# Kernel tuning notes

Hardware: AMD Instinct MI355X
Metric: run time of the kernel (lower is better)

The kernel has to match this reference:

```python
import jax, jax.numpy as jnp
import numpy as np

T, N, E = 336, 3233, 20000
FEAT, D, H = 14, 64, 128


def setup_inputs() -> dict:
    key = jax.random.key(0)
    ks = jax.random.split(key, 12)
    s = lambda k, shape, fan: jax.random.normal(k, shape, jnp.float32) / np.sqrt(fan)
    return {
        "x": jax.random.normal(ks[0], (T, N, FEAT), jnp.float32),
        "edge_index": jax.random.randint(ks[1], (2, E), 0, N, jnp.int64 if jax.config.jax_enable_x64 else jnp.int32),
        "edge_weight": jax.random.uniform(ks[2], (E,), jnp.float32),
        "W1": s(ks[3], (FEAT, D), FEAT), "b1": jnp.zeros((D,), jnp.float32),
        "W2": s(ks[4], (D, D), D), "b2": jnp.zeros((D,), jnp.float32),
        "county_bias": s(ks[5], (N, D), D),
        "W_ih": s(ks[6], (4 * H, D), D), "W_hh": s(ks[7], (4 * H, H), H),
        "b_ih": jnp.zeros((4 * H,), jnp.float32), "b_hh": jnp.zeros((4 * H,), jnp.float32),
        "Wm1": s(ks[8], (H, H // 2), H), "bm1": jnp.zeros((H // 2,), jnp.float32),
        "Wm2": s(ks[9], (H // 2, 1), H // 2), "bm2": jnp.zeros((1,), jnp.float32),
    }


def _gcn_norm(edge_index, edge_weight, n):
    # PyG GCNConv: add self-loops (weight 1) + symmetric normalization
    loop = jnp.arange(n, dtype=edge_index.dtype)
    src = jnp.concatenate([edge_index[0], loop])
    dst = jnp.concatenate([edge_index[1], loop])
    w = jnp.concatenate([edge_weight, jnp.ones((n,), edge_weight.dtype)])
    deg = jax.ops.segment_sum(w, dst, num_segments=n)
    dis = jnp.where(deg > 0, jax.lax.rsqrt(jnp.where(deg > 0, deg, 1.0)), 0.0)
    return src, dst, dis[src] * w * dis[dst]


def _gcn(h, src, dst, norm, W, b):
    # h: [T,N,Fin] -> [T,N,Fout]; transform then gather-scale-scatter over edges
    hw = jnp.einsum("tnf,fd->tnd", h, W)
    msg = hw[:, src, :] * norm[None, :, None]          # [T,E',Fout]
    out = jnp.zeros_like(hw).at[:, dst, :].add(msg)
    return out + b


def reference(x, edge_index, edge_weight, W1, b1, W2, b2, county_bias,
              W_ih, W_hh, b_ih, b_hh, Wm1, bm1, Wm2, bm2):
    n = x.shape[1]
    src, dst, norm = _gcn_norm(edge_index, edge_weight, n)
    h = jax.nn.relu(_gcn(x, src, dst, norm, W1, b1))
    embeds = _gcn(h, src, dst, norm, W2, b2) + county_bias[None]  # [T,N,D]

    hid = W_hh.shape[1]
    def step(carry, x_t):  # x_t: [N,D]
        hprev, cprev = carry
        g = x_t @ W_ih.T + hprev @ W_hh.T + (b_ih + b_hh)
        i, f, gg, o = jnp.split(g, 4, axis=-1)
        c = jax.nn.sigmoid(f) * cprev + jax.nn.sigmoid(i) * jnp.tanh(gg)
        hh = jax.nn.sigmoid(o) * jnp.tanh(c)
        return (hh, c), None

    init = (jnp.zeros((n, hid), x.dtype), jnp.zeros((n, hid), x.dtype))
    (h_final, _), _ = jax.lax.scan(step, init, embeds)
    z = jax.nn.relu(h_final @ Wm1 + bm1)
    return (z @ Wm2 + bm2)[:, 0]
```

## Files before the change

kernel.cpp:

```cpp
#include <hip/hip_runtime.h>
#include <math.h>


#define T_DIM 336
#define N_DIM 3233
#define E_DIM 20000
#define FEAT  14
#define D_DIM 64
#define H_DIM 128
#define ET    (E_DIM + N_DIM)

typedef _Float16 f16;
typedef _Float16 half8_t __attribute__((ext_vector_type(8)));
typedef _Float16 half2_t __attribute__((ext_vector_type(2)));
typedef float float4_t __attribute__((ext_vector_type(4)));

__device__ __forceinline__ float sigf(float x) {
    return __builtin_amdgcn_rcpf(1.f + exp2f(-1.4426950408889634f * x));
}
__device__ __forceinline__ float tanhfast(float x) {
    return 1.f - 2.f * __builtin_amdgcn_rcpf(1.f + exp2f(2.8853900817779268f * x));
}


__global__ void k_init(int* cnt, int* fill) {
    int i = blockIdx.x * 256 + threadIdx.x;
    if (i < N_DIM) { cnt[i] = 0; fill[i] = 0; }
}

__global__ void k_cnt(const int* __restrict__ ei, int* cnt) {
    int e = blockIdx.x * 256 + threadIdx.x;
    if (e < E_DIM) atomicAdd(&cnt[ei[E_DIM + e]], 1);
}

__global__ void k_scan(const int* __restrict__ cnt, int* __restrict__ rowp) {
    __shared__ int csum[1024];
    int tid = threadIdx.x;
    int base = tid * 4;
    int v[4];
    int s = 0;
    #pragma unroll
    for (int m = 0; m < 4; m++) {
        int idx = base + m;
        int len = (idx < N_DIM) ? (cnt[idx] + 1) : 0;
        v[m] = s; s += len;
    }
    csum[tid] = s;
    __syncthreads();
    for (int off = 1; off < 1024; off <<= 1) {
        int t2 = (tid >= off) ? csum[tid - off] : 0;
        __syncthreads();
        csum[tid] += t2;
        __syncthreads();
    }
    int pre = (tid > 0) ? csum[tid - 1] : 0;
    #pragma unroll
    for (int m = 0; m < 4; m++) {
        int idx = base + m;
        if (idx <= N_DIM) rowp[idx] = pre + v[m];
    }
}

__global__ void k_fill(const int* __restrict__ ei, const int* __restrict__ rowp,
                       int* fill, int* __restrict__ eid) {
    int e = blockIdx.x * 256 + threadIdx.x;
    if (e < ET) {
        int d = (e < E_DIM) ? ei[E_DIM + e] : (e - E_DIM);
        int p = rowp[d] + atomicAdd(&fill[d], 1);
        eid[p] = e;
    }
}

__global__ void k_sortdeg(const float* __restrict__ ew, const int* __restrict__ rowp,
                          int* __restrict__ eid, float* __restrict__ dis) {
    int n = blockIdx.x * 256 + threadIdx.x;
    if (n >= N_DIM) return;
    int p0 = rowp[n], p1 = rowp[n + 1];
    for (int i = p0 + 1; i < p1; i++) {
        int key = eid[i];
        int j = i - 1;
        while (j >= p0 && eid[j] > key) { eid[j + 1] = eid[j]; j--; }
        eid[j + 1] = key;
    }
    float deg = 0.f;
    for (int p = p0; p < p1; p++) {
        int e = eid[p];
        deg += (e < E_DIM) ? ew[e] : 1.0f;
    }
    dis[n] = rsqrtf(deg);
}

__global__ void k_csrmat(const int* __restrict__ ei, const float* __restrict__ ew,
                         const float* __restrict__ dis, const int* __restrict__ rowp,
                         const int* __restrict__ eid, int* __restrict__ csrc,
                         float* __restrict__ cnrm) {
    int n = blockIdx.x * 256 + threadIdx.x;
    if (n >= N_DIM) return;
    float dn = dis[n];
    int p0 = rowp[n], p1 = rowp[n + 1];
    for (int p = p0; p < p1; p++) {
        int e = eid[p];
        int s; float w;
        if (e < E_DIM) { s = ei[e]; w = ew[e]; }
        else           { s = e - E_DIM; w = 1.0f; }
        csrc[p] = s;
        cnrm[p] = dis[s] * w * dn;
    }
}

__global__ void k_wprep(const float* __restrict__ W2, const float* __restrict__ Wih,
                        const float* __restrict__ Whh, f16* __restrict__ wfbuf) {
    int idx = blockIdx.x * 256 + threadIdx.x;
    if (idx >= 8 * 4 * 6 * 64) return;
    int lane = idx & 63;
    int ks = (idx >> 6) % 6;
    int ct = ((idx >> 6) / 6) & 3;
    int wv = (idx >> 6) / 24;
    int q = lane >> 4, r = lane & 15;
    int g = 128 * ct + 16 * wv + r;
    f16* dst = wfbuf + (long)idx * 8;
    if (ks < 2) {
        const float* wir = Wih + (long)g * 64;
        #pragma unroll
        for (int j = 0; j < 8; j++) {
            int k = 32 * ks + 8 * q + j;
            const float* w2r = W2 + (long)k * 64;
            float s = 0.f;
            #pragma unroll 16
            for (int d = 0; d < 64; d++) s += w2r[d] * wir[d];
            dst[j] = (f16)s;
        }
    } else {
        const float* src = Whh + (long)g * 128 + 32 * (ks - 2) + 8 * q;
        #pragma unroll
        for (int j = 0; j < 8; j++) dst[j] = (f16)src[j];
    }
}

__global__ void k_gbias(const float* __restrict__ county, const float* __restrict__ b2,
                        const float* __restrict__ Wih, const float* __restrict__ bih,
                        const float* __restrict__ bhh, float* __restrict__ gbias) {
    long id = (long)blockIdx.x * 256 + threadIdx.x;
    if (id >= (long)N_DIM * 512) return;
    int n = (int)(id >> 9), g = (int)(id & 511);
    const float* wir = Wih + (long)g * 64;
    const float* cn = county + (long)n * 64;
    float s = bih[g] + bhh[g];
    #pragma unroll 16
    for (int d = 0; d < 64; d++) s += (b2[d] + cn[d]) * wir[d];
    gbias[id] = s;
}

__global__ void k_gcn1(const float* __restrict__ x, const int* __restrict__ rowp,
                       const int* __restrict__ csrc, const float* __restrict__ cnrm,
                       const float* __restrict__ W1, const float* __restrict__ b1,
                       f16* __restrict__ h, int tc) {
    __shared__ float g1[4][4][16];
    int lane = threadIdx.x & 63;
    int wv = threadIdx.x >> 6;
    long wid = ((long)blockIdx.x * 256 + threadIdx.x) >> 6;
    int ntg = (tc + 3) >> 2;
    bool wlive = wid < (long)N_DIM * ntg;

    int n = 0, tg = 0;
    if (wlive) { n = (int)(wid % N_DIM); tg = (int)(wid / N_DIM); }
    int j = lane >> 4, d = lane & 15;
    int tj = 4 * tg + j;
    bool live = wlive && (d < FEAT) && (tj < tc);

    float acc = 0.f;
    if (wlive) {
        int p0 = rowp[n], p1 = rowp[n + 1];
        for (int p = p0; p < p1; p++) {
            int s = csrc[p];
            float w = cnrm[p];
            if (live) acc += w * x[((long)tj * N_DIM + s) * FEAT + d];
        }
    }
    g1[wv][j][d] = acc;
    __syncthreads();

    if (!wlive) return;
    float wc[FEAT];
    #pragma unroll
    for (int k = 0; k < FEAT; k++) wc[k] = W1[k * 64 + lane];
    float bb = b1[lane];
    #pragma unroll
    for (int jj = 0; jj < 4; jj++) {
        int tjj = 4 * tg + jj;
        if (tjj >= tc) break;
        float a = bb;
        #pragma unroll
        for (int k = 0; k < FEAT; k++) a += g1[wv][jj][k] * wc[k];
        h[((long)tjj * N_DIM + n) * 64 + lane] = (f16)fmaxf(a, 0.f);
    }
}

__global__ void k_agg2(const f16* __restrict__ h, const int* __restrict__ rowp,
                       const int* __restrict__ csrc, const float* __restrict__ cnrm,
                       f16* __restrict__ ah, int tc) {
    int lane = threadIdx.x & 63;
    long wid = ((long)blockIdx.x * 256 + threadIdx.x) >> 6;
    int ntg = (tc + 3) >> 2;
    if (wid >= (long)N_DIM * ntg) return;
    int n = (int)(wid % N_DIM);
    int tg = (int)(wid / N_DIM);
    int tb = 4 * tg;
    int half = lane >> 5, d2 = (lane & 31) << 1;
    int ta = tb + half;
    int tbp = tb + 2 + half;
    bool la = ta < tc, lb = tbp < tc;
    float a0 = 0.f, a1 = 0.f, b0 = 0.f, b1v = 0.f;
    int p0 = rowp[n], p1 = rowp[n + 1];
    const long strideT2 = (long)2 * N_DIM * 64;
    for (int p = p0; p < p1; p++) {
        int s = csrc[p];
        float w = cnrm[p];
        const f16* base = h + ((long)ta * N_DIM + s) * 64 + d2;
        if (la) {
            half2_t va = *(const half2_t*)base;
            a0 += w * (float)va[0];
            a1 += w * (float)va[1];
        }
        if (lb) {
            half2_t vb = *(const half2_t*)(base + strideT2);
            b0  += w * (float)vb[0];
            b1v += w * (float)vb[1];
        }
    }
    f16* dst = ah + ((long)ta * N_DIM + n) * 64 + d2;
    if (la) { half2_t oa; oa[0] = (f16)a0; oa[1] = (f16)a1; *(half2_t*)dst = oa; }
    if (lb) { half2_t ob; ob[0] = (f16)b0; ob[1] = (f16)b1v; *(half2_t*)(dst + strideT2) = ob; }
}

__global__ __attribute__((amdgpu_flat_work_group_size(512, 512), amdgpu_waves_per_eu(2, 2)))
void k_lstm(
    const f16* __restrict__ ah, const f16* __restrict__ wfbuf,
    const float* __restrict__ gbias,
    const float* __restrict__ Wm1, const float* __restrict__ bm1,
    const float* __restrict__ Wm2, const float* __restrict__ bm2,
    float* __restrict__ Hst, float* __restrict__ Cst,
    int tc, int do_init, int do_head, float* __restrict__ out) {
    __shared__ __align__(16) f16   xh[2][16][136];
    __shared__ __align__(16) float hd[16][132];
    __shared__ __align__(16) float zs[16][64];

    int tid = threadIdx.x;
    int wv = tid >> 6, lane = tid & 63, q = lane >> 4, r = lane & 15;
    int nb = blockIdx.x * 16;
    int cnt = min(16, N_DIM - nb);
    int u = 16 * wv + r;

    float4_t wfr[4][6];
    #pragma unroll
    for (int ct = 0; ct < 4; ct++)
        #pragma unroll
        for (int ks = 0; ks < 6; ks++)
            wfr[ct][ks] = *(const float4_t*)&wfbuf[(long)((((wv * 4 + ct) * 6 + ks) << 6) + lane) * 8];
    #pragma unroll
    for (int ct = 0; ct < 4; ct++)
        #pragma unroll
        for (int ks = 0; ks < 6; ks++)
            asm volatile("" : "+v"(wfr[ct][ks]));

    float gb[4][4];
    #pragma unroll
    for (int reg = 0; reg < 4; reg++) {
        int node = 4 * q + reg;
        int gn = nb + node; if (gn >= N_DIM) gn = N_DIM - 1;
        #pragma unroll
        for (int ct = 0; ct < 4; ct++)
            gb[ct][reg] = gbias[(long)gn * 512 + 128 * ct + u];
    }
    #pragma unroll
    for (int ct = 0; ct < 4; ct++)
        #pragma unroll
        for (int reg = 0; reg < 4; reg++)
            asm volatile("" : "+v"(gb[ct][reg]));

    float cv[4], hvv[4];
    #pragma unroll
    for (int reg = 0; reg < 4; reg++) {
        int node = 4 * q + reg;
        bool live = (!do_init) && (node < cnt);
        hvv[reg] = live ? Hst[(long)(nb + node) * H_DIM + u] : 0.f;
        cv[reg]  = live ? Cst[(long)(nb + node) * H_DIM + u] : 0.f;
        xh[0][node][u] = (f16)hvv[reg];
    }

    int xrow = nb + r; if (xrow >= N_DIM) xrow = N_DIM - 1;
    half8_t xa = *(const half8_t*)(ah + (long)xrow * 64 + 8 * q);
    half8_t xb = *(const half8_t*)(ah + (long)xrow * 64 + 32 + 8 * q);

    int buf = 0;
    __syncthreads();

    for (int t = 0; t < tc; t++) {
        half8_t a2 = *(const half8_t*)&xh[buf][r][8 * q];
        half8_t a3 = *(const half8_t*)&xh[buf][r][32 + 8 * q];
        half8_t a4 = *(const half8_t*)&xh[buf][r][64 + 8 * q];
        half8_t a5 = *(const half8_t*)&xh[buf][r][96 + 8 * q];

        float4_t acc[4];
        #pragma unroll
        for (int ct = 0; ct < 4; ct++) {
            acc[ct][0] = gb[ct][0]; acc[ct][1] = gb[ct][1];
            acc[ct][2] = gb[ct][2]; acc[ct][3] = gb[ct][3];
        }
        #pragma unroll
        for (int ct = 0; ct < 4; ct++)
            acc[ct] = __builtin_amdgcn_mfma_f32_16x16x32_f16(xa, __builtin_bit_cast(half8_t, wfr[ct][0]), acc[ct], 0, 0, 0);
        #pragma unroll
        for (int ct = 0; ct < 4; ct++)
            acc[ct] = __builtin_amdgcn_mfma_f32_16x16x32_f16(xb, __builtin_bit_cast(half8_t, wfr[ct][1]), acc[ct], 0, 0, 0);

        int tn = (t + 1 < tc) ? t + 1 : t;
        const f16* xp = ah + ((long)tn * N_DIM + xrow) * 64;
        xa = *(const half8_t*)(xp + 8 * q);
        xb = *(const half8_t*)(xp + 32 + 8 * q);

        #pragma unroll
        for (int ct = 0; ct < 4; ct++)
            acc[ct] = __builtin_amdgcn_mfma_f32_16x16x32_f16(a2, __builtin_bit_cast(half8_t, wfr[ct][2]), acc[ct], 0, 0, 0);
        #pragma unroll
        for (int ct = 0; ct < 4; ct++)
            acc[ct] = __builtin_amdgcn_mfma_f32_16x16x32_f16(a3, __builtin_bit_cast(half8_t, wfr[ct][3]), acc[ct], 0, 0, 0);
        #pragma unroll
        for (int ct = 0; ct < 4; ct++)
            acc[ct] = __builtin_amdgcn_mfma_f32_16x16x32_f16(a4, __builtin_bit_cast(half8_t, wfr[ct][4]), acc[ct], 0, 0, 0);
        #pragma unroll
        for (int ct = 0; ct < 4; ct++)
            acc[ct] = __builtin_amdgcn_mfma_f32_16x16x32_f16(a5, __builtin_bit_cast(half8_t, wfr[ct][5]), acc[ct], 0, 0, 0);

        #pragma unroll
        for (int reg = 0; reg < 4; reg++) {
            float gi = acc[0][reg], gf = acc[1][reg], gg = acc[2][reg], go = acc[3][reg];
            float c = sigf(gf) * cv[reg] + sigf(gi) * tanhfast(gg);
            float hh = sigf(go) * tanhfast(c);
            cv[reg] = c; hvv[reg] = hh;
            xh[buf ^ 1][4 * q + reg][u] = (f16)hh;
        }
        __syncthreads();
        buf ^= 1;
    }

    #pragma unroll
    for (int reg = 0; reg < 4; reg++) {
        int node = 4 * q + reg;
        if (node < cnt) {
            Hst[(long)(nb + node) * H_DIM + u] = hvv[reg];
            Cst[(long)(nb + node) * H_DIM + u] = cv[reg];
        }
    }
    if (!do_head) return;

    #pragma unroll
    for (int reg = 0; reg < 4; reg++) hd[4 * q + reg][u] = hvv[reg];
    __syncthreads();

    for (int i = tid; i < 16 * 64; i += 512) {
        int n = i >> 6, m = i & 63;
        float a = bm1[m];
        #pragma unroll 8
        for (int k = 0; k < H_DIM; k++) a += hd[n][k] * Wm1[k * 64 + m];
        zs[n][m] = fmaxf(a, 0.f);
    }
    __syncthreads();
    if (tid < cnt) {
        float a = bm2[0];
        #pragma unroll 8
        for (int m = 0; m < 64; m++) a += zs[tid][m] * Wm2[m];
        out[nb + tid] = a;
    }
}


extern "C" void kernel_launch(void* const* d_in, const int* in_sizes, int n_in,
                              void* d_out, int out_size, void* d_ws, size_t ws_size,
                              hipStream_t stream) {
    const float* x   = (const float*)d_in[0];
    const int*   ei  = (const int*)d_in[1];
    const float* ew  = (const float*)d_in[2];
    const float* W1  = (const float*)d_in[3];
    const float* b1  = (const float*)d_in[4];
    const float* W2  = (const float*)d_in[5];
    const float* b2  = (const float*)d_in[6];
    const float* cb  = (const float*)d_in[7];
    const float* Wih = (const float*)d_in[8];
    const float* Whh = (const float*)d_in[9];
    const float* bih = (const float*)d_in[10];
    const float* bhh = (const float*)d_in[11];
    const float* Wm1 = (const float*)d_in[12];
    const float* bm1 = (const float*)d_in[13];
    const float* Wm2 = (const float*)d_in[14];
    const float* bm2 = (const float*)d_in[15];
    float* out = (float*)d_out;
    (void)in_sizes; (void)n_in; (void)out_size;

    char* ws = (char*)d_ws;
    size_t off = 0;
    auto alloc = [&](size_t bytes) -> char* {
        char* p = ws + off;
        off = (off + bytes + 255) & ~(size_t)255;
        return p;
    };
    float* dis   = (float*)alloc(N_DIM * 4);
    int*   cnt   = (int*)alloc(N_DIM * 4);
    int*   fill  = (int*)alloc(N_DIM * 4);
    int*   rowp  = (int*)alloc((N_DIM + 1) * 4);
    int*   eid   = (int*)alloc(ET * 4);
    int*   csrc  = (int*)alloc(ET * 4);
    float* cnrm  = (float*)alloc(ET * 4);
    float* Hst   = (float*)alloc((size_t)N_DIM * H_DIM * 4);
    float* Cst   = (float*)alloc((size_t)N_DIM * H_DIM * 4);
    f16*   wfbuf = (f16*)alloc((size_t)8 * 4 * 6 * 64 * 8 * 2);
    float* gbias = (float*)alloc((size_t)N_DIM * 512 * 4);

    const int cand[] = {336, 168, 112, 84, 56, 48, 28, 16, 8, 4};
    int Tc = 4;
    for (int i = 0; i < 10; i++) {
        size_t need = off + (size_t)cand[i] * N_DIM * 256 + 4096;
        if (need <= ws_size) { Tc = cand[i]; break; }
    }
    long rows = (long)Tc * N_DIM;
    f16* hbuf  = (f16*)alloc(rows * 128);
    f16* ahbuf = (f16*)alloc(rows * 128);

    k_init<<<(N_DIM + 255) / 256, 256, 0, stream>>>(cnt, fill);
    k_cnt<<<(E_DIM + 255) / 256, 256, 0, stream>>>(ei, cnt);
    k_scan<<<1, 1024, 0, stream>>>(cnt, rowp);
    k_fill<<<(ET + 255) / 256, 256, 0, stream>>>(ei, rowp, fill, eid);
    k_sortdeg<<<(N_DIM + 255) / 256, 256, 0, stream>>>(ew, rowp, eid, dis);
    k_csrmat<<<(N_DIM + 255) / 256, 256, 0, stream>>>(ei, ew, dis, rowp, eid, csrc, cnrm);
    k_wprep<<<48, 256, 0, stream>>>(W2, Wih, Whh, wfbuf);
    k_gbias<<<(int)(((long)N_DIM * 512 + 255) / 256), 256, 0, stream>>>(cb, b2, Wih, bih, bhh, gbias);

    int ntg = (Tc + 3) >> 2;
    long aggWaves = (long)N_DIM * ntg;
    int aggBlocks = (int)((aggWaves + 3) / 4);
    int lblocks   = (N_DIM + 15) / 16;
    int nChunks   = T_DIM / Tc;

    for (int c = 0; c < nChunks; c++) {
        long t0 = (long)c * Tc;
        k_gcn1<<<aggBlocks, 256, 0, stream>>>(x + t0 * N_DIM * FEAT, rowp, csrc, cnrm,
                                              W1, b1, hbuf, Tc);
        k_agg2<<<aggBlocks, 256, 0, stream>>>(hbuf, rowp, csrc, cnrm, ahbuf, Tc);
        k_lstm<<<lblocks, 512, 0, stream>>>(ahbuf, wfbuf, gbias, Wm1, bm1, Wm2, bm2,
                                            Hst, Cst, Tc, c == 0 ? 1 : 0,
                                            c == nChunks - 1 ? 1 : 0, out);
    }
}
```

Measured before the change: 1.079 ms.

## Process 32 nodes per LSTM block with 1024-thread workgroups

The LSTM kernel now handles 32 nodes per block using two groups of 8 waves, each group covering 16 nodes. Block count halves to 102 on a machine with 256 CUs, so fewer CUs are busy, while each block does twice the work per timestep. Each wave still holds its own register-resident weight fragments, and the per-step barrier now spans 16 waves instead of 8. Launch bounds change from waves_per_eu(2,2) to 1024 threads with min 1 block, which may alter register allocation.

```diff
diff --git a/kernel.cpp b/kernel.cpp
--- a/kernel.cpp
+++ b/kernel.cpp
@@ -233,30 +233,32 @@
     if (lb) { half2_t ob; ob[0] = (f16)b0; ob[1] = (f16)b1v; *(half2_t*)(dst + strideT2) = ob; }
 }
 
-__global__ __attribute__((amdgpu_flat_work_group_size(512, 512), amdgpu_waves_per_eu(2, 2)))
-void k_lstm(
+__global__ __launch_bounds__(1024, 1) void k_lstm(
     const f16* __restrict__ ah, const f16* __restrict__ wfbuf,
     const float* __restrict__ gbias,
     const float* __restrict__ Wm1, const float* __restrict__ bm1,
     const float* __restrict__ Wm2, const float* __restrict__ bm2,
     float* __restrict__ Hst, float* __restrict__ Cst,
     int tc, int do_init, int do_head, float* __restrict__ out) {
-    __shared__ __align__(16) f16   xh[2][16][136];
-    __shared__ __align__(16) float hd[16][132];
-    __shared__ __align__(16) float zs[16][64];
+    __shared__ __align__(16) f16   xh[2][32][136];
+    __shared__ __align__(16) float hd[32][132];
+    __shared__ __align__(16) float zs[32][64];
 
     int tid = threadIdx.x;
     int wv = tid >> 6, lane = tid & 63, q = lane >> 4, r = lane & 15;
-    int nb = blockIdx.x * 16;
-    int cnt = min(16, N_DIM - nb);
-    int u = 16 * wv + r;
+    int g2 = wv >> 3, wg = wv & 7;
+    int nb = blockIdx.x * 32;
+    int nbg = nb + 16 * g2;
+    int cnt32 = min(32, N_DIM - nb);
+    int u = 16 * wg + r;
+    int row0 = 16 * g2;
 
     float4_t wfr[4][6];
     #pragma unroll
     for (int ct = 0; ct < 4; ct++)
         #pragma unroll
         for (int ks = 0; ks < 6; ks++)
-            wfr[ct][ks] = *(const float4_t*)&wfbuf[(long)((((wv * 4 + ct) * 6 + ks) << 6) + lane) * 8];
+            wfr[ct][ks] = *(const float4_t*)&wfbuf[(long)((((wg * 4 + ct) * 6 + ks) << 6) + lane) * 8];
     #pragma unroll
     for (int ct = 0; ct < 4; ct++)
         #pragma unroll
@@ -266,8 +268,7 @@
     float gb[4][4];
     #pragma unroll
     for (int reg = 0; reg < 4; reg++) {
-        int node = 4 * q + reg;
-        int gn = nb + node; if (gn >= N_DIM) gn = N_DIM - 1;
+        int gn = nbg + 4 * q + reg; if (gn >= N_DIM) gn = N_DIM - 1;
         #pragma unroll
         for (int ct = 0; ct < 4; ct++)
             gb[ct][reg] = gbias[(long)gn * 512 + 128 * ct + u];
@@ -282,13 +283,14 @@
     #pragma unroll
     for (int reg = 0; reg < 4; reg++) {
         int node = 4 * q + reg;
-        bool live = (!do_init) && (node < cnt);
-        hvv[reg] = live ? Hst[(long)(nb + node) * H_DIM + u] : 0.f;
-        cv[reg]  = live ? Cst[(long)(nb + node) * H_DIM + u] : 0.f;
-        xh[0][node][u] = (f16)hvv[reg];
-    }
-
-    int xrow = nb + r; if (xrow >= N_DIM) xrow = N_DIM - 1;
+        int gn = nbg + node;
+        bool live = (!do_init) && (gn < N_DIM);
+        hvv[reg] = live ? Hst[(long)gn * H_DIM + u] : 0.f;
+        cv[reg]  = live ? Cst[(long)gn * H_DIM + u] : 0.f;
+        xh[0][row0 + node][u] = (f16)hvv[reg];
+    }
+
+    int xrow = nbg + r; if (xrow >= N_DIM) xrow = N_DIM - 1;
     half8_t xa = *(const half8_t*)(ah + (long)xrow * 64 + 8 * q);
     half8_t xb = *(const half8_t*)(ah + (long)xrow * 64 + 32 + 8 * q);
 
@@ -296,10 +298,10 @@
     __syncthreads();
 
     for (int t = 0; t < tc; t++) {
-        half8_t a2 = *(const half8_t*)&xh[buf][r][8 * q];
-        half8_t a3 = *(const half8_t*)&xh[buf][r][32 + 8 * q];
-        half8_t a4 = *(const half8_t*)&xh[buf][r][64 + 8 * q];
-        half8_t a5 = *(const half8_t*)&xh[buf][r][96 + 8 * q];
+        half8_t a2 = *(const half8_t*)&xh[buf][row0 + r][8 * q];
+        half8_t a3 = *(const half8_t*)&xh[buf][row0 + r][32 + 8 * q];
+        half8_t a4 = *(const half8_t*)&xh[buf][row0 + r][64 + 8 * q];
+        half8_t a5 = *(const half8_t*)&xh[buf][row0 + r][96 + 8 * q];
 
         float4_t acc[4];
         #pragma unroll
@@ -338,7 +340,7 @@
             float c = sigf(gf) * cv[reg] + sigf(gi) * tanhfast(gg);
             float hh = sigf(go) * tanhfast(c);
             cv[reg] = c; hvv[reg] = hh;
-            xh[buf ^ 1][4 * q + reg][u] = (f16)hh;
+            xh[buf ^ 1][row0 + 4 * q + reg][u] = (f16)hh;
         }
         __syncthreads();
         buf ^= 1;
@@ -346,19 +348,19 @@
 
     #pragma unroll
     for (int reg = 0; reg < 4; reg++) {
-        int node = 4 * q + reg;
-        if (node < cnt) {
-            Hst[(long)(nb + node) * H_DIM + u] = hvv[reg];
-            Cst[(long)(nb + node) * H_DIM + u] = cv[reg];
+        int gn = nbg + 4 * q + reg;
+        if (gn < N_DIM) {
+            Hst[(long)gn * H_DIM + u] = hvv[reg];
+            Cst[(long)gn * H_DIM + u] = cv[reg];
         }
     }
     if (!do_head) return;
 
     #pragma unroll
-    for (int reg = 0; reg < 4; reg++) hd[4 * q + reg][u] = hvv[reg];
+    for (int reg = 0; reg < 4; reg++) hd[row0 + 4 * q + reg][u] = hvv[reg];
     __syncthreads();
 
-    for (int i = tid; i < 16 * 64; i += 512) {
+    for (int i = tid; i < 32 * 64; i += 1024) {
         int n = i >> 6, m = i & 63;
         float a = bm1[m];
         #pragma unroll 8
@@ -366,7 +368,7 @@
         zs[n][m] = fmaxf(a, 0.f);
     }
     __syncthreads();
-    if (tid < cnt) {
+    if (tid < cnt32) {
         float a = bm2[0];
         #pragma unroll 8
         for (int m = 0; m < 64; m++) a += zs[tid][m] * Wm2[m];
@@ -438,7 +440,7 @@
     int ntg = (Tc + 3) >> 2;
     long aggWaves = (long)N_DIM * ntg;
     int aggBlocks = (int)((aggWaves + 3) / 4);
-    int lblocks   = (N_DIM + 15) / 16;
+    int lblocks   = (N_DIM + 31) / 32;
     int nChunks   = T_DIM / Tc;
 
     for (int c = 0; c < nChunks; c++) {
@@ -446,8 +448,8 @@
         k_gcn1<<<aggBlocks, 256, 0, stream>>>(x + t0 * N_DIM * FEAT, rowp, csrc, cnrm,
                                               W1, b1, hbuf, Tc);
         k_agg2<<<aggBlocks, 256, 0, stream>>>(hbuf, rowp, csrc, cnrm, ahbuf, Tc);
-        k_lstm<<<lblocks, 512, 0, stream>>>(ahbuf, wfbuf, gbias, Wm1, bm1, Wm2, bm2,
-                                            Hst, Cst, Tc, c == 0 ? 1 : 0,
-                                            c == nChunks - 1 ? 1 : 0, out);
-    }
-}
+        k_lstm<<<lblocks, 1024, 0, stream>>>(ahbuf, wfbuf, gbias, Wm1, bm1, Wm2, bm2,
+                                             Hst, Cst, Tc, c == 0 ? 1 : 0,
+                                             c == nChunks - 1 ? 1 : 0, out);
+    }
+}
```

Result: slower. 2.147 ms (+99.0%).
